# Performance work log

Hardware: AMD Instinct MI355X
Metric: run time of the kernel (lower is better)

Reference implementation:

```python
import jax, jax.numpy as jnp
import numpy as np
import itertools

NBX = NBY = 6
NUM_BLOCKS = NBX * NBY

def _build_adj():
    adj = []
    for i, j in itertools.product(range(NBX), range(NBY)):
        for dx, dy in [(-1, 0), (0, -1), (0, 1), (1, 0)]:
            x, y = i + dx, j + dy
            if 0 <= x < NBX and 0 <= y < NBY:
                adj.append((j * NBX + i, y * NBX + x))
    return np.array(adj, dtype=np.int32)

ADJ = _build_adj()                                   # [E=120, 2] (src, dst)
NUM_EDGES = ADJ.shape[0]
# composition structure: edge e' can be extended by edge e iff dst(e') == src(e)
COMP = (ADJ[:, 1][:, None] == ADJ[:, 0][None, :]).astype(np.float32)  # [E, E]
MAX_PATH_LEN = NUM_BLOCKS                            # 36 fixed-point iterations


def setup_inputs() -> dict:
    key = jax.random.key(0)
    ks = jax.random.split(key, 10)
    w = lambda k, shape: jax.random.normal(k, shape, jnp.float32) * 0.05
    d = {}
    d["image"] = jax.random.normal(ks[0], (1024, 1, 32, 32), jnp.float32)
    d["conv1_w"] = w(ks[1], (32, 1, 5, 5));   d["conv1_b"] = jnp.zeros((32,), jnp.float32)
    d["conv2_w"] = w(ks[2], (32, 32, 5, 5));  d["conv2_b"] = jnp.zeros((32,), jnp.float32)
    d["conv3_w"] = w(ks[3], (64, 32, 5, 5));  d["conv3_b"] = jnp.zeros((64,), jnp.float32)
    d["conv4_w"] = w(ks[4], (64, 64, 5, 5));  d["conv4_b"] = jnp.zeros((64,), jnp.float32)
    d["ep_w1"] = w(ks[5], (256, 256));        d["ep_b1"] = jnp.zeros((256,), jnp.float32)
    d["ep_w2"] = w(ks[6], (NUM_BLOCKS, 256)); d["ep_b2"] = jnp.zeros((NUM_BLOCKS,), jnp.float32)
    d["conn_w1"] = w(ks[7], (256, 256));      d["conn_b1"] = jnp.zeros((256,), jnp.float32)
    d["conn_w2"] = w(ks[8], (NUM_EDGES, 256)); d["conn_b2"] = jnp.zeros((NUM_EDGES,), jnp.float32)
    return d


def _conv(x, w, b):
    y = jax.lax.conv_general_dilated(x, w, (1, 1), 'VALID',
                                     dimension_numbers=('NCHW', 'OIHW', 'NCHW'))
    return y + b[None, :, None, None]


def _pool2(x):
    return jax.lax.reduce_window(x, -jnp.inf, jax.lax.max,
                                 (1, 1, 2, 2), (1, 1, 2, 2), 'VALID')


def reference(image, conv1_w, conv1_b, conv2_w, conv2_b, conv3_w, conv3_b,
              conv4_w, conv4_b, ep_w1, ep_b1, ep_w2, ep_b2,
              conn_w1, conn_b1, conn_w2, conn_b2):
    # --- CNN feature extractor (NCHW, torch-flatten order) ---
    x = _conv(image, conv1_w, conv1_b)      # [B,32,28,28]
    x = _conv(x, conv2_w, conv2_b)          # [B,32,24,24]
    x = _pool2(x)                           # [B,32,12,12]
    x = _conv(x, conv3_w, conv3_b)          # [B,64,8,8]
    x = _conv(x, conv4_w, conv4_b)          # [B,64,4,4]
    x = _pool2(x)                           # [B,64,2,2]
    emb = x.reshape(x.shape[0], -1)         # [B,256]

    # --- heads ---
    conn = jax.nn.sigmoid(jax.nn.relu(emb @ conn_w1.T + conn_b1) @ conn_w2.T + conn_b2)  # [B,E]
    ep = jax.nn.sigmoid(jax.nn.relu(emb @ ep_w1.T + ep_b1) @ ep_w2.T + ep_b2)            # [B,36]

    # --- recursive path building under DAMP semiring (add=clipped sum, mult=product) ---
    comp = jnp.asarray(COMP)                # [E,E]: dst(e')==src(e)
    def step(carry, _):
        old, recent = carry
        # extend_path/extend_path_cond: new symbol is the edge itself, prob = (sum_paths_ending_at_src) * p_edge
        new = jnp.clip(recent @ comp, 0.0, 1.0) * conn   # [B,E]
        merged = jnp.clip(old + new, 0.0, 1.0)           # merge (|) with DAMP add
        return (merged, new), None
    (merged, _), _ = jax.lax.scan(step, (conn, conn), None, length=MAX_PATH_LEN)

    # is_endpoint: apply_if with first_index_check / last_index_check (semiring mult)
    src = jnp.asarray(ADJ[:, 0])
    dst = jnp.asarray(ADJ[:, 1])
    paths = merged * ep[:, src] * ep[:, dst]             # [B,E]
    return paths[:, 0]
```

## Files before the change

kernel.cpp:

```cpp
#include <hip/hip_runtime.h>
#include <math.h>

typedef __attribute__((ext_vector_type(8))) short short8;
typedef __attribute__((ext_vector_type(4))) float float4v;
typedef __attribute__((ext_vector_type(4))) unsigned short ushort4v;

static __device__ __forceinline__ unsigned short f2bf(float f) {
    union { float f; unsigned u; } v; v.f = f;
    unsigned u = v.u;
    return (unsigned short)((u + 0x7fffu + ((u >> 16) & 1u)) >> 16);
}
static __device__ __forceinline__ unsigned pk2(float a, float b) {
    return (unsigned)f2bf(a) | ((unsigned)f2bf(b) << 16);
}

struct AdjT {
    int src[120];
    int dst[120];
    int cnt[36];
    int idx[36][4];
    int ostart[36];
    int ocnt[36];
};

constexpr AdjT build_adj() {
    AdjT a{};
    const int ddx[4] = {-1, 0, 0, 1};
    const int ddy[4] = {0, -1, 1, 0};
    int ne = 0;
    for (int i = 0; i < 6; i++)
        for (int j = 0; j < 6; j++)
            for (int d = 0; d < 4; d++) {
                int x = i + ddx[d], y = j + ddy[d];
                if (x >= 0 && x < 6 && y >= 0 && y < 6) {
                    a.src[ne] = j * 6 + i;
                    a.dst[ne] = y * 6 + x;
                    ne++;
                }
            }
    for (int n = 0; n < 36; n++) {
        a.cnt[n] = 0;
        for (int e = 0; e < 120; e++)
            if (a.dst[e] == n) a.idx[n][a.cnt[n]++] = e;
    }
    for (int n = 0; n < 36; n++) { a.ostart[n] = 0; a.ocnt[n] = 0; }
    for (int e = 0; e < 120; e++) {
        a.ocnt[a.src[e]]++;
        if (e == 0 || a.src[e] != a.src[e - 1]) a.ostart[a.src[e]] = e;
    }
    return a;
}

__device__ constexpr AdjT ADJC = build_adj();
__device__ constexpr int G16_START[17] =
    {0, 3, 6, 9, 12, 14, 16, 18, 20, 22, 24, 26, 28, 30, 32, 34, 36};

__global__ __launch_bounds__(256) void k_prepall(
    const float* __restrict__ w1, const float* __restrict__ b1,
    const float* __restrict__ w2, const float* __restrict__ b2,
    const float* __restrict__ w3, const float* __restrict__ w4,
    const float* __restrict__ cnw1, const float* __restrict__ epw1,
    const float* __restrict__ cnw2, const float* __restrict__ epw2,
    unsigned short* __restrict__ wpc, float* __restrict__ wcb,
    unsigned short* __restrict__ wp3, unsigned short* __restrict__ wp4,
    unsigned short* __restrict__ wph1, unsigned short* __restrict__ wpcn2,
    unsigned short* __restrict__ wpep2) {
    __shared__ float s_w1[800];
    __shared__ float s_w2[800];
    if (blockIdx.x < 32) {
        const int co = blockIdx.x, tid = threadIdx.x;
        for (int i = tid; i < 800; i += 256) {
            s_w1[i] = w1[i];
            s_w2[i] = w2[co * 800 + i];
        }
        __syncthreads();
        if (tid < 128) {
            int t = tid;
            int ty = t / 12, tx = t - 12 * ty;
            float val = 0.f;
            if (ty < 9 && tx < 9) {
                int ylo = ty > 4 ? ty - 4 : 0, yhi = ty < 4 ? ty : 4;
                int xlo = tx > 4 ? tx - 4 : 0, xhi = tx < 4 ? tx : 4;
                for (int k1y = ylo; k1y <= yhi; k1y++)
                    for (int k1x = xlo; k1x <= xhi; k1x++) {
                        int o1 = k1y * 5 + k1x;
                        int o2 = (ty - k1y) * 5 + (tx - k1x);
#pragma unroll
                        for (int ci = 0; ci < 32; ci++)
                            val += s_w1[ci * 25 + o1] * s_w2[ci * 25 + o2];
                    }
            }
            int n = co >> 1, nt = co & 1;
            int ks = t >> 5, r = t & 31, q = r >> 3, j = r & 7;
            wpc[ks * 1024 + nt * 512 + (q * 16 + n) * 8 + j] = f2bf(val);
        } else if (tid == 128) {
            float s = b2[co];
            for (int ci = 0; ci < 32; ci++) {
                float ws = 0.f;
#pragma unroll
                for (int t2 = 0; t2 < 25; t2++) ws += s_w2[ci * 25 + t2];
                s += b1[ci] * ws;
            }
            wcb[co] = s;
        }
        return;
    }
    int e = (blockIdx.x - 32) * 256 + threadIdx.x;
    if (e < 51200) {
        int j = e & 7, lane = (e >> 3) & 63, nt = (e >> 9) & 3, t = e >> 11;
        int co = 4 * (lane & 15) + nt, ci = (lane >> 4) * 8 + j;
        wp3[e] = f2bf(w3[(co * 32 + ci) * 25 + t]);
    } else if (e < 153600) {
        int e4 = e - 51200;
        int j = e4 & 7, lane = (e4 >> 3) & 63, nt = (e4 >> 9) & 3;
        int ks = (e4 >> 11) & 1, t = e4 >> 12;
        int co = 4 * (lane & 15) + nt, ci = ks * 32 + (lane >> 4) * 8 + j;
        wp4[e4] = f2bf(w4[(co * 64 + ci) * 25 + t]);
    } else {
        int eh = e - 153600;
        if (eh < 131072) {
            int j = eh & 7, lane = (eh >> 3) & 63, nt = (eh >> 9) & 31, kt = eh >> 14;
            int c = nt * 16 + (lane & 15);
            int k = kt * 32 + ((lane >> 4) << 3) + j;
            float v = (c < 256) ? cnw1[c * 256 + k] : epw1[(c - 256) * 256 + k];
            wph1[eh] = f2bf(v);
        } else if (eh < 163840) {
            int e2 = eh - 131072;
            int j = e2 & 7, lane = (e2 >> 3) & 63, nt = (e2 >> 9) & 7, kt = e2 >> 12;
            int c = nt * 16 + (lane & 15);
            int k = kt * 32 + ((lane >> 4) << 3) + j;
            wpcn2[e2] = f2bf(c < 120 ? cnw2[c * 256 + k] : 0.f);
        } else {
            int e3 = eh - 163840;
            int j = e3 & 7, lane = (e3 >> 3) & 63, idx = e3 >> 9;
            int kt = idx / 3, nt = idx - kt * 3;
            int c = nt * 16 + (lane & 15);
            int k = kt * 32 + ((lane >> 4) << 3) + j;
            wpep2[e3] = f2bf(c < 36 ? epw2[c * 256 + k] : 0.f);
        }
    }
}

#define REGSZ 10656
#define C3O 5760
#define CPY 1224

__global__ __launch_bounds__(512) void k_convall(
    const float* __restrict__ img,
    const unsigned short* __restrict__ wpc, const float* __restrict__ wcb,
    const unsigned short* __restrict__ wp3, const float* __restrict__ b3,
    const unsigned short* __restrict__ wp4, const float* __restrict__ b4,
    unsigned short* __restrict__ emb) {
    __shared__ __align__(16) unsigned short s_buf[2 * REGSZ];
    const int b2 = blockIdx.x, tid = threadIdx.x;
    const int lane = tid & 63, wave = tid >> 6;
    const int m = lane & 15, quad = lane >> 4;

    {
        int simg = tid >> 8, t = tid & 255;
        float4 v = ((const float4*)(img + (size_t)(2 * b2 + simg) * 1024))[t];
        unsigned short pv[4];
        pv[0] = f2bf(v.x); pv[1] = f2bf(v.y);
        pv[2] = f2bf(v.z); pv[3] = f2bf(v.w);
        int r = t >> 3, x0 = (t & 7) * 4;
        int p36 = r * 36 + x0;
        unsigned short* reg = s_buf + simg * REGSZ + C3O;
#pragma unroll
        for (int c = 0; c < 4; c++)
#pragma unroll
            for (int i = 0; i < 4; i++) {
                int pos = p36 + i - c;
                if (pos >= 0) reg[c * CPY + pos] = pv[i];
            }
    }
    if (tid < 400) {
        int simg = tid >= 200, zz = tid - 200 * simg;
        int r, x;
        if (zz < 128) { r = zz >> 2; x = 32 + (zz & 3); }
        else { int rr = zz - 128; r = 32 + (rr >= 36 ? 1 : 0); x = rr - (rr >= 36 ? 36 : 0); }
        int p36 = r * 36 + x;
        unsigned short* reg = s_buf + simg * REGSZ + C3O;
#pragma unroll
        for (int c = 0; c < 4; c++) {
            int pos = p36 - c;
            if (pos >= 0 && pos < CPY) reg[c * CPY + pos] = 0;
        }
    }

    const short8* wqc = (const short8*)wpc;
    short8 cb0[4], cb1[4];
#pragma unroll
    for (int ks = 0; ks < 4; ks++) {
        cb0[ks] = wqc[(ks * 2 + 0) * 64 + lane];
        cb1[ks] = wqc[(ks * 2 + 1) * 64 + lane];
    }
    const float bc0 = wcb[2 * m], bc1 = wcb[2 * m + 1];
    int ct1[4], ct2[4];
#pragma unroll
    for (int ks = 0; ks < 4; ks++) {
        int t0 = ks * 32 + quad * 8;
        ct1[ks] = (t0 / 12) * 36 + (t0 % 12);
        int t4 = t0 + 4;
        ct2[ks] = (t4 / 12) * 36 + (t4 % 12);
    }
    const short8* wq3 = (const short8*)wp3;

    __syncthreads();

    for (int TT = wave; TT < 72; TT += 8) {
        int ci = TT >= 36 ? 1 : 0;
        int T = TT - 36 * ci;
        int pg = T * 4 + (m >> 2);
        int py = (pg * 171) >> 11;
        int px = pg - py * 12;
        int albase = (2 * py + ((m & 3) >> 1)) * 36 + 2 * px + (m & 1);
        const unsigned short* reg = s_buf + ci * REGSZ + C3O;
        float4v a0 = {0.f, 0.f, 0.f, 0.f};
        float4v a1 = {0.f, 0.f, 0.f, 0.f};
#pragma unroll
        for (int ks = 0; ks < 4; ks++) {
            int a = albase + ct1[ks];
            int c = a & 3;
            ushort4v lo = *(const ushort4v*)(reg + c * CPY + (a - c));
            a = albase + ct2[ks];
            c = a & 3;
            ushort4v hi = *(const ushort4v*)(reg + c * CPY + (a - c));
            short8 av;
            av[0] = (short)lo[0]; av[1] = (short)lo[1];
            av[2] = (short)lo[2]; av[3] = (short)lo[3];
            av[4] = (short)hi[0]; av[5] = (short)hi[1];
            av[6] = (short)hi[2]; av[7] = (short)hi[3];
            a0 = __builtin_amdgcn_mfma_f32_16x16x32_bf16(av, cb0[ks], a0, 0, 0, 0);
            a1 = __builtin_amdgcn_mfma_f32_16x16x32_bf16(av, cb1[ks], a1, 0, 0, 0);
        }
        float mx0 = fmaxf(fmaxf(a0[0], a0[1]), fmaxf(a0[2], a0[3])) + bc0;
        float mx1 = fmaxf(fmaxf(a1[0], a1[1]), fmaxf(a1[2], a1[3])) + bc1;
        int row = T * 4 + quad;
        *(unsigned*)(s_buf + ci * REGSZ + row * 40 + 2 * m) = pk2(mx0, mx1);
    }
    __syncthreads();

    {
        const int img3 = wave >> 2;
        const int mt0 = ((wave >> 1) & 1) * 2;
        const int nt0 = (wave & 1) * 2;
        const unsigned short* sb = s_buf + img3 * REGSZ;
        int a3[2];
#pragma unroll
        for (int mi = 0; mi < 2; mi++) {
            int pos3 = (mt0 + mi) * 16 + m;
            int y3 = pos3 >> 3, x3 = pos3 & 7;
            a3[mi] = (y3 * 12 + x3) * 40 + quad * 8;
        }
        float4v acc3[2][2];
#pragma unroll
        for (int mi = 0; mi < 2; mi++)
#pragma unroll
            for (int ni = 0; ni < 2; ni++)
                acc3[mi][ni] = (float4v){0.f, 0.f, 0.f, 0.f};
        short8 bw3[2];
        bw3[0] = wq3[nt0 * 64 + lane];
        bw3[1] = wq3[(nt0 + 1) * 64 + lane];
        for (int t = 0; t < 25; t++) {
            short8 nb3[2];
            if (t < 24) {
                nb3[0] = wq3[((t + 1) * 4 + nt0) * 64 + lane];
                nb3[1] = wq3[((t + 1) * 4 + nt0 + 1) * 64 + lane];
            }
            const int ky = t / 5, kx = t - ky * 5;
            const int toff = (ky * 12 + kx) * 40;
            short8 av0 = *(const short8*)(sb + a3[0] + toff);
            short8 av1 = *(const short8*)(sb + a3[1] + toff);
            acc3[0][0] = __builtin_amdgcn_mfma_f32_16x16x32_bf16(av0, bw3[0], acc3[0][0], 0, 0, 0);
            acc3[0][1] = __builtin_amdgcn_mfma_f32_16x16x32_bf16(av0, bw3[1], acc3[0][1], 0, 0, 0);
            acc3[1][0] = __builtin_amdgcn_mfma_f32_16x16x32_bf16(av1, bw3[0], acc3[1][0], 0, 0, 0);
            acc3[1][1] = __builtin_amdgcn_mfma_f32_16x16x32_bf16(av1, bw3[1], acc3[1][1], 0, 0, 0);
            if (t < 24) { bw3[0] = nb3[0]; bw3[1] = nb3[1]; }
        }
        float bb0 = b3[4 * m + nt0], bb1 = b3[4 * m + nt0 + 1];
#pragma unroll
        for (int mi = 0; mi < 2; mi++)
#pragma unroll
            for (int r = 0; r < 4; r++) {
                int row3 = (mt0 + mi) * 16 + quad * 4 + r;
                *(unsigned*)(s_buf + img3 * REGSZ + C3O + row3 * 72 + 4 * m + nt0) =
                    pk2(acc3[mi][0][r] + bb0, acc3[mi][1][r] + bb1);
            }
    }
    __syncthreads();

    {
        const int img4 = wave >> 2, nt4 = wave & 3;
        int y4 = m >> 2, x4 = m & 3;
        const unsigned short* sb = s_buf + img4 * REGSZ;
        int a4 = C3O + (y4 * 8 + x4) * 72 + quad * 8;
        float4v acc4 = (float4v){0.f, 0.f, 0.f, 0.f};
        const short8* wq4 = (const short8*)wp4;
        short8 cw0 = wq4[(0 * 4 + nt4) * 64 + lane];
        short8 cw1 = wq4[(1 * 4 + nt4) * 64 + lane];
        for (int t = 0; t < 25; t++) {
            short8 n0, n1;
            if (t < 24) {
                n0 = wq4[(((t + 1) * 2) * 4 + nt4) * 64 + lane];
                n1 = wq4[(((t + 1) * 2 + 1) * 4 + nt4) * 64 + lane];
            }
            const int ky = t / 5, kx = t - ky * 5;
            const int toff = (ky * 8 + kx) * 72;
            short8 av0 = *(const short8*)(sb + a4 + toff);
            acc4 = __builtin_amdgcn_mfma_f32_16x16x32_bf16(av0, cw0, acc4, 0, 0, 0);
            short8 av1 = *(const short8*)(sb + a4 + toff + 32);
            acc4 = __builtin_amdgcn_mfma_f32_16x16x32_bf16(av1, cw1, acc4, 0, 0, 0);
            if (t < 24) { cw0 = n0; cw1 = n1; }
        }
        float* s_c4 = (float*)(s_buf + img4 * REGSZ);
#pragma unroll
        for (int r = 0; r < 4; r++)
            s_c4[(quad * 4 + r) * 68 + 4 * m + nt4] = acc4[r];
    }
    __syncthreads();

    {
        const int simg = tid >> 8, t = tid & 255;
        const float* s_c4 = (const float*)(s_buf + simg * REGSZ);
        int co = t >> 2, pp = t & 3;
        int ppy = pp >> 1, ppx = pp & 1;
        float v0 = s_c4[((2 * ppy) * 4 + 2 * ppx) * 68 + co];
        float v1 = s_c4[((2 * ppy) * 4 + 2 * ppx + 1) * 68 + co];
        float v2 = s_c4[((2 * ppy + 1) * 4 + 2 * ppx) * 68 + co];
        float v3 = s_c4[((2 * ppy + 1) * 4 + 2 * ppx + 1) * 68 + co];
        emb[(size_t)(2 * b2 + simg) * 256 + t] =
            f2bf(fmaxf(fmaxf(v0, v1), fmaxf(v2, v3)) + b4[co]);
    }
}

__global__ __launch_bounds__(256) void k_heads(
    const unsigned short* __restrict__ emb,
    const unsigned short* __restrict__ wph1,
    const float* __restrict__ cn_b1, const float* __restrict__ ep_b1,
    const unsigned short* __restrict__ wpcn2, const float* __restrict__ cn_b2,
    const unsigned short* __restrict__ wpep2, const float* __restrict__ ep_b2,
    float* __restrict__ out) {
    __shared__ unsigned short s_hid[16 * 520];
    __shared__ float s_conn[120 * 17];
    __shared__ float s_rec0[120 * 17];
    __shared__ float s_rec1[120 * 17];
    __shared__ float s_ep[36 * 17];
    const int tid = threadIdx.x;
    const int lane = tid & 63, wave = tid >> 6;
    const int m = lane & 15, q = lane >> 4;
    const int b0 = blockIdx.x * 16;

    float4v acc[8];
#pragma unroll
    for (int i = 0; i < 8; i++) acc[i] = (float4v){0.f, 0.f, 0.f, 0.f};
    const short8* wp1 = (const short8*)wph1;
    for (int kt = 0; kt < 8; kt++) {
        short8 av = *(const short8*)(emb + (size_t)(b0 + m) * 256 + kt * 32 + q * 8);
#pragma unroll
        for (int ntl = 0; ntl < 8; ntl++) {
            int nt = wave * 8 + ntl;
            short8 bv = wp1[(kt * 32 + nt) * 64 + lane];
            acc[ntl] = __builtin_amdgcn_mfma_f32_16x16x32_bf16(av, bv, acc[ntl], 0, 0, 0);
        }
    }
#pragma unroll
    for (int ntl = 0; ntl < 8; ntl++) {
        int c = (wave * 8 + ntl) * 16 + m;
        float bb = (c < 256) ? cn_b1[c] : ep_b1[c - 256];
#pragma unroll
        for (int r = 0; r < 4; r++)
            s_hid[(q * 4 + r) * 520 + c] = f2bf(fmaxf(acc[ntl][r] + bb, 0.f));
    }
    __syncthreads();

    for (int job = wave; job < 11; job += 4) {
        const bool isconn = job < 8;
        const int koff = isconn ? 0 : 256;
        float4v a2 = (float4v){0.f, 0.f, 0.f, 0.f};
        for (int kt = 0; kt < 8; kt++) {
            short8 av = *(const short8*)(s_hid + m * 520 + koff + kt * 32 + q * 8);
            short8 bv = isconn
                ? ((const short8*)wpcn2)[(kt * 8 + job) * 64 + lane]
                : ((const short8*)wpep2)[(kt * 3 + (job - 8)) * 64 + lane];
            a2 = __builtin_amdgcn_mfma_f32_16x16x32_bf16(av, bv, a2, 0, 0, 0);
        }
        int c = (isconn ? job : (job - 8)) * 16 + m;
        float bb = isconn ? (c < 120 ? cn_b2[c] : 0.f) : (c < 36 ? ep_b2[c] : 0.f);
#pragma unroll
        for (int r = 0; r < 4; r++) {
            float v = 1.f / (1.f + __expf(-(a2[r] + bb)));
            int row = q * 4 + r;
            if (isconn) {
                if (c < 120) { s_conn[c * 17 + row] = v; s_rec0[c * 17 + row] = v; }
            } else {
                if (c < 36) s_ep[c * 17 + row] = v;
            }
        }
    }
    __syncthreads();

    const int row = tid >> 4, g = tid & 15;
    const int ns = G16_START[g];
    const int nodecnt = G16_START[g + 1] - ns;
    int ie[3][4], icnt[3], os[3], oc[3];
    float cr[3][4];
#pragma unroll
    for (int s = 0; s < 3; s++) {
        if (s < nodecnt) {
            int n = ns + s;
            icnt[s] = ADJC.cnt[n];
#pragma unroll
            for (int qx = 0; qx < 4; qx++) ie[s][qx] = ADJC.idx[n][qx];
            os[s] = ADJC.ostart[n];
            oc[s] = ADJC.ocnt[n];
#pragma unroll
            for (int oe = 0; oe < 4; oe++)
                cr[s][oe] = (oe < oc[s]) ? s_conn[(os[s] + oe) * 17 + row] : 0.f;
        } else {
            icnt[s] = 0; oc[s] = 0; os[s] = 0;
#pragma unroll
            for (int qx = 0; qx < 4; qx++) ie[s][qx] = 0;
#pragma unroll
            for (int oe = 0; oe < 4; oe++) cr[s][oe] = 0.f;
        }
    }
    float old0 = (g == 0) ? s_conn[0 * 17 + row] : 0.f;

    for (int it = 0; it < 36; it++) {
        const float* cur = (it & 1) ? s_rec1 : s_rec0;
        float* nxt = (it & 1) ? s_rec0 : s_rec1;
#pragma unroll
        for (int s = 0; s < 3; s++) {
            float sum = 0.f;
#pragma unroll
            for (int qx = 0; qx < 4; qx++)
                sum += (qx < icnt[s]) ? cur[ie[s][qx] * 17 + row] : 0.f;
            sum = fminf(sum, 1.f);
#pragma unroll
            for (int oe = 0; oe < 4; oe++) {
                if (oe < oc[s]) {
                    int e = os[s] + oe;
                    float nv = sum * cr[s][oe];
                    nxt[e * 17 + row] = nv;
                    if (g == 0 && s == 0 && oe == 0)
                        old0 = fminf(old0 + nv, 1.f);
                }
            }
        }
        __asm__ volatile("s_waitcnt lgkmcnt(0)" ::: "memory");
    }

    if (g == 0)
        out[b0 + row] = old0 * s_ep[0 * 17 + row] * s_ep[6 * 17 + row];
}

extern "C" void kernel_launch(void* const* d_in, const int* in_sizes, int n_in,
                              void* d_out, int out_size, void* d_ws, size_t ws_size,
                              hipStream_t stream) {
    const float* image = (const float*)d_in[0];
    const float* c1w = (const float*)d_in[1];
    const float* c1b = (const float*)d_in[2];
    const float* c2w = (const float*)d_in[3];
    const float* c2b = (const float*)d_in[4];
    const float* c3w = (const float*)d_in[5];
    const float* c3b = (const float*)d_in[6];
    const float* c4w = (const float*)d_in[7];
    const float* c4b = (const float*)d_in[8];
    const float* epw1 = (const float*)d_in[9];
    const float* epb1 = (const float*)d_in[10];
    const float* epw2 = (const float*)d_in[11];
    const float* epb2 = (const float*)d_in[12];
    const float* cnw1 = (const float*)d_in[13];
    const float* cnb1 = (const float*)d_in[14];
    const float* cnw2 = (const float*)d_in[15];
    const float* cnb2 = (const float*)d_in[16];

    const int B = in_sizes[0] / (32 * 32);

    unsigned short* ws = (unsigned short*)d_ws;
    unsigned short* embo = ws;
    unsigned short* wp3 = embo + (size_t)B * 256;
    unsigned short* wp4 = wp3 + 51200;
    unsigned short* wph1 = wp4 + 102400;
    unsigned short* wpcn2 = wph1 + 131072;
    unsigned short* wpep2 = wpcn2 + 32768;
    unsigned short* wpc = wpep2 + 12288;
    float* wcb = (float*)(wpc + 4096);

    k_prepall<<<1320, 256, 0, stream>>>(c1w, c1b, c2w, c2b, c3w, c4w,
                                        cnw1, epw1, cnw2, epw2,
                                        wpc, wcb, wp3, wp4, wph1, wpcn2, wpep2);
    k_convall<<<B / 2, 512, 0, stream>>>(image, wpc, wcb, wp3, c3b, wp4, c4b, embo);
    k_heads<<<B / 16, 256, 0, stream>>>(embo, wph1, cnb1, epb1,
                                        wpcn2, cnb2, wpep2, epb2, (float*)d_out);
}
```

Measured before the change: 161.6 us.

## Recast path fixed-point as per-node wave-shuffle recurrence with one wave per sample

The 36-step path propagation now runs as a per-node recurrence on the clipped sum of incoming edge values. One wave handles one batch row and one lane handles one node. Neighbour values are exchanged with wave shuffles, which removes the double-buffered shared-memory edge arrays and the per-iteration LDS traffic. The heads kernel is widened to 1024 threads so each wave does fewer MFMA tiles and one second-layer job. The cost is larger blocks with lower occupancy per CU, and k_heads is probably a small share of total time anyway.

```diff
diff --git a/kernel.cpp b/kernel.cpp
--- a/kernel.cpp
+++ b/kernel.cpp
@@ -52,8 +52,6 @@
 }
 
 __device__ constexpr AdjT ADJC = build_adj();
-__device__ constexpr int G16_START[17] =
-    {0, 3, 6, 9, 12, 14, 16, 18, 20, 22, 24, 26, 28, 30, 32, 34, 36};
 
 __global__ __launch_bounds__(256) void k_prepall(
     const float* __restrict__ w1, const float* __restrict__ b1,
@@ -333,7 +331,7 @@
     }
 }
 
-__global__ __launch_bounds__(256) void k_heads(
+__global__ __launch_bounds__(1024) void k_heads(
     const unsigned short* __restrict__ emb,
     const unsigned short* __restrict__ wph1,
     const float* __restrict__ cn_b1, const float* __restrict__ ep_b1,
@@ -342,30 +340,28 @@
     float* __restrict__ out) {
     __shared__ unsigned short s_hid[16 * 520];
     __shared__ float s_conn[120 * 17];
-    __shared__ float s_rec0[120 * 17];
-    __shared__ float s_rec1[120 * 17];
     __shared__ float s_ep[36 * 17];
     const int tid = threadIdx.x;
     const int lane = tid & 63, wave = tid >> 6;
     const int m = lane & 15, q = lane >> 4;
     const int b0 = blockIdx.x * 16;
 
-    float4v acc[8];
-#pragma unroll
-    for (int i = 0; i < 8; i++) acc[i] = (float4v){0.f, 0.f, 0.f, 0.f};
+    float4v acc[2];
+    acc[0] = (float4v){0.f, 0.f, 0.f, 0.f};
+    acc[1] = (float4v){0.f, 0.f, 0.f, 0.f};
     const short8* wp1 = (const short8*)wph1;
     for (int kt = 0; kt < 8; kt++) {
         short8 av = *(const short8*)(emb + (size_t)(b0 + m) * 256 + kt * 32 + q * 8);
 #pragma unroll
-        for (int ntl = 0; ntl < 8; ntl++) {
-            int nt = wave * 8 + ntl;
+        for (int ntl = 0; ntl < 2; ntl++) {
+            int nt = wave * 2 + ntl;
             short8 bv = wp1[(kt * 32 + nt) * 64 + lane];
             acc[ntl] = __builtin_amdgcn_mfma_f32_16x16x32_bf16(av, bv, acc[ntl], 0, 0, 0);
         }
     }
 #pragma unroll
-    for (int ntl = 0; ntl < 8; ntl++) {
-        int c = (wave * 8 + ntl) * 16 + m;
+    for (int ntl = 0; ntl < 2; ntl++) {
+        int c = (wave * 2 + ntl) * 16 + m;
         float bb = (c < 256) ? cn_b1[c] : ep_b1[c - 256];
 #pragma unroll
         for (int r = 0; r < 4; r++)
@@ -373,7 +369,8 @@
     }
     __syncthreads();
 
-    for (int job = wave; job < 11; job += 4) {
+    if (wave < 11) {
+        const int job = wave;
         const bool isconn = job < 8;
         const int koff = isconn ? 0 : 256;
         float4v a2 = (float4v){0.f, 0.f, 0.f, 0.f};
@@ -391,7 +388,7 @@
             float v = 1.f / (1.f + __expf(-(a2[r] + bb)));
             int row = q * 4 + r;
             if (isconn) {
-                if (c < 120) { s_conn[c * 17 + row] = v; s_rec0[c * 17 + row] = v; }
+                if (c < 120) s_conn[c * 17 + row] = v;
             } else {
                 if (c < 36) s_ep[c * 17 + row] = v;
             }
@@ -399,59 +396,38 @@
     }
     __syncthreads();
 
-    const int row = tid >> 4, g = tid & 15;
-    const int ns = G16_START[g];
-    const int nodecnt = G16_START[g + 1] - ns;
-    int ie[3][4], icnt[3], os[3], oc[3];
-    float cr[3][4];
-#pragma unroll
-    for (int s = 0; s < 3; s++) {
-        if (s < nodecnt) {
-            int n = ns + s;
-            icnt[s] = ADJC.cnt[n];
-#pragma unroll
-            for (int qx = 0; qx < 4; qx++) ie[s][qx] = ADJC.idx[n][qx];
-            os[s] = ADJC.ostart[n];
-            oc[s] = ADJC.ocnt[n];
-#pragma unroll
-            for (int oe = 0; oe < 4; oe++)
-                cr[s][oe] = (oe < oc[s]) ? s_conn[(os[s] + oe) * 17 + row] : 0.f;
-        } else {
-            icnt[s] = 0; oc[s] = 0; os[s] = 0;
-#pragma unroll
-            for (int qx = 0; qx < 4; qx++) ie[s][qx] = 0;
-#pragma unroll
-            for (int oe = 0; oe < 4; oe++) cr[s][oe] = 0.f;
-        }
-    }
-    float old0 = (g == 0) ? s_conn[0 * 17 + row] : 0.f;
-
-    for (int it = 0; it < 36; it++) {
-        const float* cur = (it & 1) ? s_rec1 : s_rec0;
-        float* nxt = (it & 1) ? s_rec0 : s_rec1;
-#pragma unroll
-        for (int s = 0; s < 3; s++) {
-            float sum = 0.f;
-#pragma unroll
-            for (int qx = 0; qx < 4; qx++)
-                sum += (qx < icnt[s]) ? cur[ie[s][qx] * 17 + row] : 0.f;
-            sum = fminf(sum, 1.f);
-#pragma unroll
-            for (int oe = 0; oe < 4; oe++) {
-                if (oe < oc[s]) {
-                    int e = os[s] + oe;
-                    float nv = sum * cr[s][oe];
-                    nxt[e * 17 + row] = nv;
-                    if (g == 0 && s == 0 && oe == 0)
-                        old0 = fminf(old0 + nv, 1.f);
-                }
-            }
-        }
-        __asm__ volatile("s_waitcnt lgkmcnt(0)" ::: "memory");
-    }
-
-    if (g == 0)
-        out[b0 + row] = old0 * s_ep[0 * 17 + row] * s_ep[6 * 17 + row];
+    {
+        const int w = wave;
+        const int n = lane;
+        int msrc[4];
+        float cr[4];
+        const int cnt = (n < 36) ? ADJC.cnt[n] : 0;
+#pragma unroll
+        for (int k = 0; k < 4; k++) {
+            if (n < 36 && k < cnt) {
+                int e = ADJC.idx[n][k];
+                msrc[k] = ADJC.src[e];
+                cr[k] = s_conn[e * 17 + w];
+            } else {
+                msrc[k] = 0;
+                cr[k] = 0.f;
+            }
+        }
+        float S = fminf(cr[0] + cr[1] + cr[2] + cr[3], 1.f);
+        const float conn0 = s_conn[0 * 17 + w];
+        float old0 = conn0;
+        for (int it = 0; it < 36; it++) {
+            float s0 = __shfl(S, 0);
+            float g0 = __shfl(S, msrc[0]);
+            float g1 = __shfl(S, msrc[1]);
+            float g2 = __shfl(S, msrc[2]);
+            float g3 = __shfl(S, msrc[3]);
+            old0 = fminf(old0 + s0 * conn0, 1.f);
+            S = fminf(g0 * cr[0] + g1 * cr[1] + g2 * cr[2] + g3 * cr[3], 1.f);
+        }
+        if (lane == 0)
+            out[b0 + w] = old0 * s_ep[0 * 17 + w] * s_ep[6 * 17 + w];
+    }
 }
 
 extern "C" void kernel_launch(void* const* d_in, const int* in_sizes, int n_in,
@@ -491,6 +467,6 @@
                                         cnw1, epw1, cnw2, epw2,
                                         wpc, wcb, wp3, wp4, wph1, wpcn2, wpep2);
     k_convall<<<B / 2, 512, 0, stream>>>(image, wpc, wcb, wp3, c3b, wp4, c4b, embo);
-    k_heads<<<B / 16, 256, 0, stream>>>(embo, wph1, cnb1, epb1,
-                                        wpcn2, cnb2, wpep2, epb2, (float*)d_out);
-}
+    k_heads<<<B / 16, 1024, 0, stream>>>(embo, wph1, cnb1, epb1,
+                                         wpcn2, cnb2, wpep2, epb2, (float*)d_out);
+}
```

New measurement: 142.8 us. 11.7% less time.
